# Optimization experiments

Hardware: AMD Instinct MI355X
Metric: run time of the kernel (lower is better)

Reference implementation:

```python
import jax, jax.numpy as jnp
import numpy as np

B, D, C = 8192, 2048, 1000
EPS32 = float(np.finfo(np.float32).eps)      # torch clamp_probs uses finfo.eps
LOG_2PI = float(np.log(2.0 * np.pi))
GAMMA = float(1.0 / np.exp(100.0))           # lerp at global_step=0 -> start_val = 1/exp(start_rho)


def setup_inputs() -> dict:
    key = jax.random.key(0)
    k = jax.random.split(key, 6)
    feature = jax.random.normal(k[0], (B, D), jnp.float32)
    target = jax.random.randint(k[1], (B,), 0, C)
    eps = jax.random.normal(k[2], (B, D), jnp.float32)
    # y_project: Linear(C, D) -> weight [D, C], bias [D]
    y_w = jax.random.normal(k[3], (D, C), jnp.float32) * 0.02
    y_b = jnp.zeros((D,), jnp.float32)
    # cls_project: Linear(D, C) -> weight [C, D], bias [C]
    # small weights + positive bias keep Categorical probs positive (torch would
    # clamp negatives to eps; we replicate the clamp but avoid degenerate NaNs)
    cls_w = jax.random.normal(k[4], (C, D), jnp.float32) * 0.001
    cls_b = jnp.ones((C,), jnp.float32) * 5.0
    return dict(feature=feature, y_w=y_w, y_b=y_b, cls_w=cls_w, cls_b=cls_b,
                eps=eps, target=target)


def reference(feature, y_w, y_b, cls_w, cls_b, eps, target):
    # z = m.sample() : identity-covariance MVN sample, detached (torch .sample())
    z = jax.lax.stop_gradient(feature + eps)                      # [B, D]

    # y_emb = y_project(one_hot(target)) == gather of weight columns + bias
    y_emb = jnp.take(y_w, target, axis=1).T + y_b                 # [B, D]

    # Categorical(probs=cls_project(z)): normalize, clamp, log
    probs_raw = z @ cls_w.T + cls_b                               # [B, C]
    p = probs_raw / jnp.sum(probs_raw, axis=-1, keepdims=True)
    logits = jnp.log(jnp.clip(p, EPS32, 1.0 - EPS32))             # [B, C]

    # identity-covariance MVN log_prob in closed form
    const = 0.5 * D * LOG_2PI
    h1 = 0.5 * jnp.sum((z - feature) ** 2, axis=-1) + const       # -m.log_prob(z)
    h2 = 0.5 * jnp.sum((z - y_emb) ** 2, axis=-1) + const         # -y_emb_d.log_prob(z)
    h3 = -jnp.take_along_axis(logits, target[:, None], axis=1)[:, 0]

    rex = h2 - h1
    loss = jnp.mean(jnp.float32(GAMMA) * rex + h3)
    return logits, loss
```

## Files before the change

kernel.cpp:

```cpp
#include <hip/hip_runtime.h>
#include <hip/hip_bf16.h>

#define B_ROWS 8192
#define D_DIM  2048
#define C_DIM  1000
#define C_PAD  1024

#define EPS32   1.1920928955078125e-07f

typedef __attribute__((ext_vector_type(8))) short short8;
typedef __attribute__((ext_vector_type(4))) float f32x4;

#define GLOAD_LDS16(gptr, lptr) \
  __builtin_amdgcn_global_load_lds((const __attribute__((address_space(1))) void*)(gptr), \
                                   (__attribute__((address_space(3))) void*)(lptr), 16, 0, 0)

__device__ inline unsigned short f2bf(float x) {
  union { __hip_bfloat16 b; unsigned short u; } cv;
  cv.b = __float2bfloat16(x);
  return cv.u;
}

__device__ inline float wave_red(float v) {
#pragma unroll
  for (int off = 32; off > 0; off >>= 1) v += __shfl_down(v, off, 64);
  return v;
}

__global__ __launch_bounds__(256) void fuse_z(const float4* __restrict__ f4,
                                              const float4* __restrict__ e4,
                                              uint2* __restrict__ z,
                                              const float* __restrict__ cls_w,
                                              __hip_bfloat16* __restrict__ clsw_bf) {
  int bid = blockIdx.x;
  if (bid < 16384) {
    int i = bid * 256 + threadIdx.x;
    float4 f = f4[i];
    float4 e = e4[i];
    union { unsigned short u[4]; uint2 v; } pz;
    pz.u[0] = f2bf(f.x + e.x);
    pz.u[1] = f2bf(f.y + e.y);
    pz.u[2] = f2bf(f.z + e.z);
    pz.u[3] = f2bf(f.w + e.w);
    z[i] = pz.v;
  } else {
    int j = ((bid - 16384) * 256 + threadIdx.x) * 8;
    int row = j >> 11;
    int col = j & 2047;
    union { unsigned short u[8]; uint4 v; } pk;
    if (row < C_DIM) {
      const float* src = cls_w + (size_t)row * D_DIM + col;
#pragma unroll
      for (int i2 = 0; i2 < 8; ++i2) pk.u[i2] = f2bf(src[i2]);
    } else {
#pragma unroll
      for (int i2 = 0; i2 < 8; ++i2) pk.u[i2] = 0;
    }
    *(uint4*)((unsigned short*)clsw_bf + j) = pk.v;
  }
}

__global__ __launch_bounds__(256) void gemm_bt(const __hip_bfloat16* __restrict__ A,
                                               const __hip_bfloat16* __restrict__ Bt,
                                               const float* __restrict__ cls_b,
                                               float* __restrict__ out) {
  __shared__ __align__(16) __hip_bfloat16 sA[128 * 64];
  __shared__ __align__(16) __hip_bfloat16 sB[128 * 64];
  const int tid = threadIdx.x;
  const int m0 = blockIdx.x * 128;
  const int n0 = blockIdx.y * 128;
  const int w = tid >> 6, lane = tid & 63;
  const int wm = (w & 1) * 64, wn = (w >> 1) * 64;
  const int l15 = lane & 15, quad = lane >> 4;

  f32x4 acc[4][4] = {};

  for (int k0 = 0; k0 < D_DIM; k0 += 64) {
#pragma unroll
    for (int i = 0; i < 4; ++i) {
      int j = i * 256 + tid;
      int row = j >> 3;
      int cc = (j & 7) ^ (row & 7);
      const __hip_bfloat16* srcA = A + (size_t)(m0 + row) * D_DIM + k0 + cc * 8;
      const __hip_bfloat16* srcB = Bt + (size_t)(n0 + row) * D_DIM + k0 + cc * 8;
      GLOAD_LDS16(srcA, &sA[j * 8]);
      GLOAD_LDS16(srcB, &sB[j * 8]);
    }
    __syncthreads();
#pragma unroll
    for (int kk = 0; kk < 64; kk += 32) {
      const int ccr = (kk >> 3) + quad;
      short8 af[4], bfr[4];
#pragma unroll
      for (int i = 0; i < 4; ++i) {
        int r = wm + i * 16 + l15;
        af[i] = *(const short8*)&sA[(r * 8 + (ccr ^ (r & 7))) * 8];
      }
#pragma unroll
      for (int jn = 0; jn < 4; ++jn) {
        int r = wn + jn * 16 + l15;
        bfr[jn] = *(const short8*)&sB[(r * 8 + (ccr ^ (r & 7))) * 8];
      }
#pragma unroll
      for (int i = 0; i < 4; ++i)
#pragma unroll
        for (int jn = 0; jn < 4; ++jn)
          acc[i][jn] = __builtin_amdgcn_mfma_f32_16x16x32_bf16(af[i], bfr[jn], acc[i][jn], 0, 0, 0);
    }
    __syncthreads();
  }

#pragma unroll
  for (int i = 0; i < 4; ++i) {
    int row = m0 + wm + i * 16 + quad * 4;
#pragma unroll
    for (int jn = 0; jn < 4; ++jn) {
      int col = n0 + wn + jn * 16 + l15;
      if (col < C_DIM) {
        float bias = cls_b[col];
#pragma unroll
        for (int r = 0; r < 4; ++r)
          out[(size_t)(row + r) * C_DIM + col] = acc[i][jn][r] + bias;
      }
    }
  }
}

__global__ __launch_bounds__(256) void rownorm(float* __restrict__ out,
                                               const int* __restrict__ target,
                                               float* __restrict__ rowloss) {
  int b = blockIdx.x * 4 + (threadIdx.x >> 6);
  int lane = threadIdx.x & 63;
  float* row = out + (size_t)b * C_DIM;

  float v[16];
  float s = 0.f;
#pragma unroll
  for (int k = 0; k < 4; ++k) {
    int c = k * 256 + lane * 4;
    if (c + 3 < C_DIM) {
      float4 f = *(const float4*)(row + c);
      v[k * 4 + 0] = f.x; v[k * 4 + 1] = f.y; v[k * 4 + 2] = f.z; v[k * 4 + 3] = f.w;
    } else {
#pragma unroll
      for (int i = 0; i < 4; ++i) v[k * 4 + i] = (c + i < C_DIM) ? row[c + i] : 0.f;
    }
    s += v[k * 4 + 0] + v[k * 4 + 1] + v[k * 4 + 2] + v[k * 4 + 3];
  }
  s = wave_red(s);
  float inv = 1.0f / __shfl(s, 0, 64);
  int t = target[b];

#pragma unroll
  for (int k = 0; k < 4; ++k) {
    int c = k * 256 + lane * 4;
    float lg[4];
#pragma unroll
    for (int i = 0; i < 4; ++i) {
      float p = v[k * 4 + i] * inv;
      p = fminf(fmaxf(p, EPS32), 1.0f - EPS32);
      lg[i] = __logf(p);
      if (c + i == t) rowloss[b] = -lg[i];
    }
    if (c + 3 < C_DIM) {
      *(float4*)(row + c) = make_float4(lg[0], lg[1], lg[2], lg[3]);
    } else {
#pragma unroll
      for (int i = 0; i < 4; ++i) if (c + i < C_DIM) row[c + i] = lg[i];
    }
  }
}

__global__ __launch_bounds__(256) void finalize(const float* __restrict__ rowloss,
                                                float* __restrict__ out_loss) {
  int tid = threadIdx.x;
  float s = 0.f;
  for (int i = tid; i < B_ROWS; i += 256) s += rowloss[i];
  s = wave_red(s);
  __shared__ float sm[4];
  if ((tid & 63) == 0) sm[tid >> 6] = s;
  __syncthreads();
  if (tid == 0) out_loss[0] = (sm[0] + sm[1] + sm[2] + sm[3]) * (1.0f / B_ROWS);
}

extern "C" void kernel_launch(void* const* d_in, const int* in_sizes, int n_in,
                              void* d_out, int out_size, void* d_ws, size_t ws_size,
                              hipStream_t stream) {
  const float* feature = (const float*)d_in[0];
  const float* cls_w   = (const float*)d_in[3];
  const float* cls_b   = (const float*)d_in[4];
  const float* eps     = (const float*)d_in[5];
  const int*   target  = (const int*)d_in[6];
  float* out = (float*)d_out;
  float* out_loss = out + (size_t)B_ROWS * C_DIM;

  char* ws = (char*)d_ws;
  __hip_bfloat16* z_bf    = (__hip_bfloat16*)ws;
  __hip_bfloat16* clsw_bf = (__hip_bfloat16*)(ws + 33554432);
  float*          rowloss = (float*)(ws + 33554432 + 4194304);

  fuse_z<<<dim3(16384 + 1024), 256, 0, stream>>>((const float4*)feature, (const float4*)eps,
                                                 (uint2*)z_bf, cls_w, clsw_bf);
  gemm_bt<<<dim3(B_ROWS / 128, C_PAD / 128), 256, 0, stream>>>(z_bf, clsw_bf, cls_b, out);
  rownorm<<<dim3(B_ROWS / 4), 256, 0, stream>>>(out, target, rowloss);
  finalize<<<dim3(1), 256, 0, stream>>>(rowloss, out_loss);
}
```

Baseline: 237.3 us.

## Fuse z computation and bf16 conversion into GEMM loads, merge finalize into rownorm

```diff
diff --git a/kernel.cpp b/kernel.cpp
--- a/kernel.cpp
+++ b/kernel.cpp
@@ -11,10 +11,6 @@
 typedef __attribute__((ext_vector_type(8))) short short8;
 typedef __attribute__((ext_vector_type(4))) float f32x4;
 
-#define GLOAD_LDS16(gptr, lptr) \
-  __builtin_amdgcn_global_load_lds((const __attribute__((address_space(1))) void*)(gptr), \
-                                   (__attribute__((address_space(3))) void*)(lptr), 16, 0, 0)
-
 __device__ inline unsigned short f2bf(float x) {
   union { __hip_bfloat16 b; unsigned short u; } cv;
   cv.b = __float2bfloat16(x);
@@ -27,48 +23,18 @@
   return v;
 }
 
-__global__ __launch_bounds__(256) void fuse_z(const float4* __restrict__ f4,
-                                              const float4* __restrict__ e4,
-                                              uint2* __restrict__ z,
-                                              const float* __restrict__ cls_w,
-                                              __hip_bfloat16* __restrict__ clsw_bf) {
-  int bid = blockIdx.x;
-  if (bid < 16384) {
-    int i = bid * 256 + threadIdx.x;
-    float4 f = f4[i];
-    float4 e = e4[i];
-    union { unsigned short u[4]; uint2 v; } pz;
-    pz.u[0] = f2bf(f.x + e.x);
-    pz.u[1] = f2bf(f.y + e.y);
-    pz.u[2] = f2bf(f.z + e.z);
-    pz.u[3] = f2bf(f.w + e.w);
-    z[i] = pz.v;
-  } else {
-    int j = ((bid - 16384) * 256 + threadIdx.x) * 8;
-    int row = j >> 11;
-    int col = j & 2047;
-    union { unsigned short u[8]; uint4 v; } pk;
-    if (row < C_DIM) {
-      const float* src = cls_w + (size_t)row * D_DIM + col;
-#pragma unroll
-      for (int i2 = 0; i2 < 8; ++i2) pk.u[i2] = f2bf(src[i2]);
-    } else {
-#pragma unroll
-      for (int i2 = 0; i2 < 8; ++i2) pk.u[i2] = 0;
-    }
-    *(uint4*)((unsigned short*)clsw_bf + j) = pk.v;
-  }
-}
-
-__global__ __launch_bounds__(256) void gemm_bt(const __hip_bfloat16* __restrict__ A,
-                                               const __hip_bfloat16* __restrict__ Bt,
-                                               const float* __restrict__ cls_b,
-                                               float* __restrict__ out) {
+__global__ __launch_bounds__(256, 2) void gemm_fused(const float* __restrict__ feature,
+                                                     const float* __restrict__ eps,
+                                                     const float* __restrict__ cls_w,
+                                                     const float* __restrict__ cls_b,
+                                                     float* __restrict__ out,
+                                                     unsigned int* __restrict__ counter) {
   __shared__ __align__(16) __hip_bfloat16 sA[128 * 64];
   __shared__ __align__(16) __hip_bfloat16 sB[128 * 64];
   const int tid = threadIdx.x;
-  const int m0 = blockIdx.x * 128;
-  const int n0 = blockIdx.y * 128;
+  const int n0 = blockIdx.x * 128;
+  const int m0 = blockIdx.y * 128;
+  if (blockIdx.x == 0 && blockIdx.y == 0 && tid == 0) *counter = 0;
   const int w = tid >> 6, lane = tid & 63;
   const int wm = (w & 1) * 64, wn = (w >> 1) * 64;
   const int l15 = lane & 15, quad = lane >> 4;
@@ -79,12 +45,33 @@
 #pragma unroll
     for (int i = 0; i < 4; ++i) {
       int j = i * 256 + tid;
-      int row = j >> 3;
-      int cc = (j & 7) ^ (row & 7);
-      const __hip_bfloat16* srcA = A + (size_t)(m0 + row) * D_DIM + k0 + cc * 8;
-      const __hip_bfloat16* srcB = Bt + (size_t)(n0 + row) * D_DIM + k0 + cc * 8;
-      GLOAD_LDS16(srcA, &sA[j * 8]);
-      GLOAD_LDS16(srcB, &sB[j * 8]);
+      int row = j >> 3, cc = j & 7;
+      const float4* fp = (const float4*)(feature + (size_t)(m0 + row) * D_DIM + k0 + cc * 8);
+      const float4* ep = (const float4*)(eps + (size_t)(m0 + row) * D_DIM + k0 + cc * 8);
+      float4 f0 = fp[0], f1 = fp[1];
+      float4 e0 = ep[0], e1 = ep[1];
+      union { unsigned short u[8]; uint4 v; } pk;
+      pk.u[0] = f2bf(f0.x + e0.x); pk.u[1] = f2bf(f0.y + e0.y);
+      pk.u[2] = f2bf(f0.z + e0.z); pk.u[3] = f2bf(f0.w + e0.w);
+      pk.u[4] = f2bf(f1.x + e1.x); pk.u[5] = f2bf(f1.y + e1.y);
+      pk.u[6] = f2bf(f1.z + e1.z); pk.u[7] = f2bf(f1.w + e1.w);
+      *(uint4*)&sA[(row * 8 + (cc ^ (row & 7))) * 8] = pk.v;
+    }
+#pragma unroll
+    for (int i = 0; i < 4; ++i) {
+      int j = i * 256 + tid;
+      int row = j >> 3, cc = j & 7;
+      int gr = n0 + row;
+      union { unsigned short u[8]; uint4 v; } pk;
+      if (gr < C_DIM) {
+        const float4* bp = (const float4*)(cls_w + (size_t)gr * D_DIM + k0 + cc * 8);
+        float4 b0 = bp[0], b1 = bp[1];
+        pk.u[0] = f2bf(b0.x); pk.u[1] = f2bf(b0.y); pk.u[2] = f2bf(b0.z); pk.u[3] = f2bf(b0.w);
+        pk.u[4] = f2bf(b1.x); pk.u[5] = f2bf(b1.y); pk.u[6] = f2bf(b1.z); pk.u[7] = f2bf(b1.w);
+      } else {
+        pk.v = make_uint4(0, 0, 0, 0);
+      }
+      *(uint4*)&sB[(row * 8 + (cc ^ (row & 7))) * 8] = pk.v;
     }
     __syncthreads();
 #pragma unroll
@@ -126,10 +113,13 @@
   }
 }
 
-__global__ __launch_bounds__(256) void rownorm(float* __restrict__ out,
-                                               const int* __restrict__ target,
-                                               float* __restrict__ rowloss) {
-  int b = blockIdx.x * 4 + (threadIdx.x >> 6);
+__global__ __launch_bounds__(256) void rownorm_final(float* __restrict__ out,
+                                                     const int* __restrict__ target,
+                                                     float* __restrict__ partial,
+                                                     unsigned int* __restrict__ counter,
+                                                     float* __restrict__ out_loss) {
+  int bid = blockIdx.x;
+  int b = bid * 4 + (threadIdx.x >> 6);
   int lane = threadIdx.x & 63;
   float* row = out + (size_t)b * C_DIM;
 
@@ -151,6 +141,7 @@
   float inv = 1.0f / __shfl(s, 0, 64);
   int t = target[b];
 
+  float h3c = 0.f;
 #pragma unroll
   for (int k = 0; k < 4; ++k) {
     int c = k * 256 + lane * 4;
@@ -160,7 +151,7 @@
       float p = v[k * 4 + i] * inv;
       p = fminf(fmaxf(p, EPS32), 1.0f - EPS32);
       lg[i] = __logf(p);
-      if (c + i == t) rowloss[b] = -lg[i];
+      if (c + i == t) h3c = -lg[i];
     }
     if (c + 3 < C_DIM) {
       *(float4*)(row + c) = make_float4(lg[0], lg[1], lg[2], lg[3]);
@@ -169,18 +160,31 @@
       for (int i = 0; i < 4; ++i) if (c + i < C_DIM) row[c + i] = lg[i];
     }
   }
-}
-
-__global__ __launch_bounds__(256) void finalize(const float* __restrict__ rowloss,
-                                                float* __restrict__ out_loss) {
-  int tid = threadIdx.x;
-  float s = 0.f;
-  for (int i = tid; i < B_ROWS; i += 256) s += rowloss[i];
-  s = wave_red(s);
-  __shared__ float sm[4];
-  if ((tid & 63) == 0) sm[tid >> 6] = s;
+
+  float h3 = wave_red(h3c);
+  __shared__ float wsum[4];
+  __shared__ bool is_last;
+  int w = threadIdx.x >> 6;
+  if (lane == 0) wsum[w] = h3;
   __syncthreads();
-  if (tid == 0) out_loss[0] = (sm[0] + sm[1] + sm[2] + sm[3]) * (1.0f / B_ROWS);
+  if (threadIdx.x == 0) {
+    partial[bid] = wsum[0] + wsum[1] + wsum[2] + wsum[3];
+    __threadfence();
+    unsigned int ticket = atomicAdd(counter, 1u);
+    is_last = (ticket == gridDim.x - 1);
+  }
+  __syncthreads();
+  if (is_last) {
+    __threadfence();
+    float s2 = 0.f;
+#pragma unroll
+    for (int k = 0; k < 8; ++k) s2 += partial[threadIdx.x + k * 256];
+    s2 = wave_red(s2);
+    if (lane == 0) wsum[w] = s2;
+    __syncthreads();
+    if (threadIdx.x == 0)
+      out_loss[0] = (wsum[0] + wsum[1] + wsum[2] + wsum[3]) * (1.0f / B_ROWS);
+  }
 }
 
 extern "C" void kernel_launch(void* const* d_in, const int* in_sizes, int n_in,
@@ -195,13 +199,10 @@
   float* out_loss = out + (size_t)B_ROWS * C_DIM;
 
   char* ws = (char*)d_ws;
-  __hip_bfloat16* z_bf    = (__hip_bfloat16*)ws;
-  __hip_bfloat16* clsw_bf = (__hip_bfloat16*)(ws + 33554432);
-  float*          rowloss = (float*)(ws + 33554432 + 4194304);
-
-  fuse_z<<<dim3(16384 + 1024), 256, 0, stream>>>((const float4*)feature, (const float4*)eps,
-                                                 (uint2*)z_bf, cls_w, clsw_bf);
-  gemm_bt<<<dim3(B_ROWS / 128, C_PAD / 128), 256, 0, stream>>>(z_bf, clsw_bf, cls_b, out);
-  rownorm<<<dim3(B_ROWS / 4), 256, 0, stream>>>(out, target, rowloss);
-  finalize<<<dim3(1), 256, 0, stream>>>(rowloss, out_loss);
-}
+  float*        partial = (float*)ws;
+  unsigned int* counter = (unsigned int*)(ws + 8192);
+
+  gemm_fused<<<dim3(C_PAD / 128, B_ROWS / 128), 256, 0, stream>>>(feature, eps, cls_w, cls_b,
+                                                                  out, counter);
+  rownorm_final<<<dim3(B_ROWS / 4), 256, 0, stream>>>(out, target, partial, counter, out_loss);
+}
```

Result: slower. 428.2 us (+80.5%).

## Fuse row normalization and loss reduction into GEMM via last-block strip tickets

Applied to the files above, without the earlier changes.

```diff
diff --git a/kernel.cpp b/kernel.cpp
--- a/kernel.cpp
+++ b/kernel.cpp
@@ -31,7 +31,8 @@
                                               const float4* __restrict__ e4,
                                               uint2* __restrict__ z,
                                               const float* __restrict__ cls_w,
-                                              __hip_bfloat16* __restrict__ clsw_bf) {
+                                              __hip_bfloat16* __restrict__ clsw_bf,
+                                              unsigned int* __restrict__ strip_cnt) {
   int bid = blockIdx.x;
   if (bid < 16384) {
     int i = bid * 256 + threadIdx.x;
@@ -44,6 +45,7 @@
     pz.u[3] = f2bf(f.w + e.w);
     z[i] = pz.v;
   } else {
+    if (bid == 16384 && threadIdx.x < 66) strip_cnt[threadIdx.x] = 0;
     int j = ((bid - 16384) * 256 + threadIdx.x) * 8;
     int row = j >> 11;
     int col = j & 2047;
@@ -60,10 +62,14 @@
   }
 }
 
-__global__ __launch_bounds__(256) void gemm_bt(const __hip_bfloat16* __restrict__ A,
-                                               const __hip_bfloat16* __restrict__ Bt,
-                                               const float* __restrict__ cls_b,
-                                               float* __restrict__ out) {
+__global__ __launch_bounds__(256) void gemm_fused(const __hip_bfloat16* __restrict__ A,
+                                                  const __hip_bfloat16* __restrict__ Bt,
+                                                  const float* __restrict__ cls_b,
+                                                  const int* __restrict__ target,
+                                                  float* __restrict__ out,
+                                                  unsigned int* __restrict__ strip_cnt,
+                                                  float* __restrict__ strip_h3,
+                                                  float* __restrict__ out_loss) {
   __shared__ __align__(16) __hip_bfloat16 sA[128 * 64];
   __shared__ __align__(16) __hip_bfloat16 sB[128 * 64];
   const int tid = threadIdx.x;
@@ -124,63 +130,70 @@
       }
     }
   }
-}
-
-__global__ __launch_bounds__(256) void rownorm(float* __restrict__ out,
-                                               const int* __restrict__ target,
-                                               float* __restrict__ rowloss) {
-  int b = blockIdx.x * 4 + (threadIdx.x >> 6);
-  int lane = threadIdx.x & 63;
-  float* row = out + (size_t)b * C_DIM;
-
-  float v[16];
-  float s = 0.f;
-#pragma unroll
-  for (int k = 0; k < 4; ++k) {
-    int c = k * 256 + lane * 4;
-    if (c + 3 < C_DIM) {
-      float4 f = *(const float4*)(row + c);
-      v[k * 4 + 0] = f.x; v[k * 4 + 1] = f.y; v[k * 4 + 2] = f.z; v[k * 4 + 3] = f.w;
-    } else {
-#pragma unroll
-      for (int i = 0; i < 4; ++i) v[k * 4 + i] = (c + i < C_DIM) ? row[c + i] : 0.f;
-    }
-    s += v[k * 4 + 0] + v[k * 4 + 1] + v[k * 4 + 2] + v[k * 4 + 3];
-  }
-  s = wave_red(s);
-  float inv = 1.0f / __shfl(s, 0, 64);
-  int t = target[b];
-
-#pragma unroll
-  for (int k = 0; k < 4; ++k) {
-    int c = k * 256 + lane * 4;
-    float lg[4];
-#pragma unroll
-    for (int i = 0; i < 4; ++i) {
-      float p = v[k * 4 + i] * inv;
-      p = fminf(fmaxf(p, EPS32), 1.0f - EPS32);
-      lg[i] = __logf(p);
-      if (c + i == t) rowloss[b] = -lg[i];
-    }
-    if (c + 3 < C_DIM) {
-      *(float4*)(row + c) = make_float4(lg[0], lg[1], lg[2], lg[3]);
-    } else {
-#pragma unroll
-      for (int i = 0; i < 4; ++i) if (c + i < C_DIM) row[c + i] = lg[i];
-    }
-  }
-}
-
-__global__ __launch_bounds__(256) void finalize(const float* __restrict__ rowloss,
-                                                float* __restrict__ out_loss) {
-  int tid = threadIdx.x;
-  float s = 0.f;
-  for (int i = tid; i < B_ROWS; i += 256) s += rowloss[i];
-  s = wave_red(s);
-  __shared__ float sm[4];
-  if ((tid & 63) == 0) sm[tid >> 6] = s;
+
+  __threadfence();
+  __shared__ unsigned int ticket_s;
+  if (tid == 0) ticket_s = atomicAdd(&strip_cnt[blockIdx.x], 1u);
   __syncthreads();
-  if (tid == 0) out_loss[0] = (sm[0] + sm[1] + sm[2] + sm[3]) * (1.0f / B_ROWS);
+  if (ticket_s != 7) return;
+  __threadfence();
+
+  float h3w = 0.f;
+  for (int rr = 0; rr < 32; ++rr) {
+    int b = m0 + w * 32 + rr;
+    float* row = out + (size_t)b * C_DIM;
+    float v[16];
+    float s = 0.f;
+#pragma unroll
+    for (int k = 0; k < 4; ++k) {
+      int c = k * 256 + lane * 4;
+      if (c + 3 < C_DIM) {
+        float4 f = *(const float4*)(row + c);
+        v[k * 4 + 0] = f.x; v[k * 4 + 1] = f.y; v[k * 4 + 2] = f.z; v[k * 4 + 3] = f.w;
+      } else {
+#pragma unroll
+        for (int i = 0; i < 4; ++i) v[k * 4 + i] = (c + i < C_DIM) ? row[c + i] : 0.f;
+      }
+      s += v[k * 4 + 0] + v[k * 4 + 1] + v[k * 4 + 2] + v[k * 4 + 3];
+    }
+    s = wave_red(s);
+    float inv = 1.0f / __shfl(s, 0, 64);
+    int t = target[b];
+#pragma unroll
+    for (int k = 0; k < 4; ++k) {
+      int c = k * 256 + lane * 4;
+      float lg[4];
+#pragma unroll
+      for (int i = 0; i < 4; ++i) {
+        float p = v[k * 4 + i] * inv;
+        p = fminf(fmaxf(p, EPS32), 1.0f - EPS32);
+        lg[i] = __logf(p);
+        if (c + i == t) h3w += -lg[i];
+      }
+      if (c + 3 < C_DIM) {
+        *(float4*)(row + c) = make_float4(lg[0], lg[1], lg[2], lg[3]);
+      } else {
+#pragma unroll
+        for (int i = 0; i < 4; ++i) if (c + i < C_DIM) row[c + i] = lg[i];
+      }
+    }
+  }
+
+  h3w = wave_red(h3w);
+  __shared__ float hsum[4];
+  if (lane == 0) hsum[w] = h3w;
+  __syncthreads();
+  if (tid == 0) {
+    strip_h3[blockIdx.x] = hsum[0] + hsum[1] + hsum[2] + hsum[3];
+    __threadfence();
+    unsigned int t2 = atomicAdd(&strip_cnt[64], 1u);
+    if (t2 == 63) {
+      __threadfence();
+      float s = 0.f;
+      for (int i = 0; i < 64; ++i) s += strip_h3[i];
+      out_loss[0] = s * (1.0f / B_ROWS);
+    }
+  }
 }
 
 extern "C" void kernel_launch(void* const* d_in, const int* in_sizes, int n_in,
@@ -195,13 +208,13 @@
   float* out_loss = out + (size_t)B_ROWS * C_DIM;
 
   char* ws = (char*)d_ws;
-  __hip_bfloat16* z_bf    = (__hip_bfloat16*)ws;
-  __hip_bfloat16* clsw_bf = (__hip_bfloat16*)(ws + 33554432);
-  float*          rowloss = (float*)(ws + 33554432 + 4194304);
+  __hip_bfloat16* z_bf      = (__hip_bfloat16*)ws;
+  __hip_bfloat16* clsw_bf   = (__hip_bfloat16*)(ws + 33554432);
+  unsigned int*   strip_cnt = (unsigned int*)(ws + 37748736);
+  float*          strip_h3  = (float*)(ws + 37749248);
 
   fuse_z<<<dim3(16384 + 1024), 256, 0, stream>>>((const float4*)feature, (const float4*)eps,
-                                                 (uint2*)z_bf, cls_w, clsw_bf);
-  gemm_bt<<<dim3(B_ROWS / 128, C_PAD / 128), 256, 0, stream>>>(z_bf, clsw_bf, cls_b, out);
-  rownorm<<<dim3(B_ROWS / 4), 256, 0, stream>>>(out, target, rowloss);
-  finalize<<<dim3(1), 256, 0, stream>>>(rowloss, out_loss);
-}
+                                                 (uint2*)z_bf, cls_w, clsw_bf, strip_cnt);
+  gemm_fused<<<dim3(B_ROWS / 128, C_PAD / 128), 256, 0, stream>>>(z_bf, clsw_bf, cls_b, target,
+                                                                  out, strip_cnt, strip_h3, out_loss);
+}
```

Measured after the change: 338.1 us. 1.42x slower.
